# Performance work log

Hardware: AMD Instinct MI355X
Metric: run time of the kernel (lower is better)

Reference implementation:

```python
import jax, jax.numpy as jnp
import numpy as np
from jax import lax

LBDA = 0.5   # soft-min temperature from OTAM_cum_dist_v2 default
EPS = 0.01   # cos_sim epsilon


def otam_cum_dist(dists, lbda=LBDA):
    """Soft-DTW-style OTAM DP. dists: [nq, ns, L, S] -> [nq, ns].
    Faithful to OTAM_cum_dist_v2: pad last dim by (1,1) with zeros, then run the
    row-wise recurrence. Soft-min computed via stable logsumexp (same math as
    -lbda*log(sum exp(-x/lbda)))."""
    nq, ns, L, S = dists.shape
    d = jnp.pad(dists, ((0, 0), (0, 0), (0, 0), (1, 1)))  # [nq, ns, L, W], W=S+2
    W = S + 2
    # Row 0: cum[0, m] = cum[0, m-1] + d[0, m], cum[0, 0] = 0
    row0 = jnp.concatenate(
        [jnp.zeros((nq, ns, 1), d.dtype), jnp.cumsum(d[:, :, 0, 1:], axis=-1)], axis=-1)
    if L == 1:
        return row0[..., -1]

    m_idx = jnp.arange(1, W)
    include_up = (m_idx == 1) | (m_idx == W - 1)  # only first/last cols use cum[l-1, m]
    INF = jnp.asarray(jnp.inf, d.dtype)

    def row_step(prev_row, d_row):
        # prev_row, d_row: [nq, ns, W]
        xs = (
            jnp.moveaxis(d_row[:, :, 1:], -1, 0),        # d[l, m],       [W-1, nq, ns]
            jnp.moveaxis(prev_row[:, :, :-1], -1, 0),    # cum[l-1, m-1]
            jnp.moveaxis(prev_row[:, :, 1:], -1, 0),     # cum[l-1, m]
            include_up,
        )

        def col_step(cur_left, x):
            d_m, p_diag, p_up, inc = x
            up = jnp.where(inc, p_up, INF)               # masked term -> exp(-inf)=0
            terms = jnp.stack([p_diag, cur_left, up])    # [3, nq, ns]
            new = d_m - lbda * jax.nn.logsumexp(-terms / lbda, axis=0)
            return new, new

        _, cols = lax.scan(col_step, jnp.zeros((nq, ns), d.dtype), xs)
        row = jnp.concatenate(
            [jnp.zeros((nq, ns, 1), d.dtype), jnp.moveaxis(cols, 0, -1)], axis=-1)
        return row, None

    d_rows = jnp.moveaxis(d[:, :, 1:, :], 2, 0)          # [L-1, nq, ns, W]
    final_row, _ = lax.scan(row_step, row0, d_rows)
    return final_row[..., -1]


def reference(support_features, query_features):
    """OTAM meta-logits (cum_dist_g = -otam_distance) of DSN_TEMPORAL.
    support_features: [n_classes, L, D] class prototypes; query_features: [nq, L, D]."""
    nq, Lq, D = query_features.shape
    ns, Ls, _ = support_features.shape
    q = query_features.reshape(nq * Lq, D)
    s = support_features.reshape(ns * Ls, D)
    # cos_sim with epsilon in denominator (faithful to cos_sim())
    num = q @ s.T
    den = (jnp.linalg.norm(q, axis=-1)[:, None]
           * jnp.linalg.norm(s, axis=-1)[None, :] + EPS)
    frame_dists = 1.0 - num / den                         # [nq*L, ns*S]
    dists = frame_dists.reshape(nq, Lq, ns, Ls).transpose(0, 2, 1, 3)  # [nq, ns, L, S]
    cum = otam_cum_dist(dists) + otam_cum_dist(dists.transpose(0, 1, 3, 2))
    return -cum                                           # meta_logits [nq, ns]


def setup_inputs() -> dict:
    key = jax.random.key(0)
    k1, k2 = jax.random.split(key)
    return {
        "support_features": jax.random.normal(k1, (64, 8, 576), dtype=jnp.float32),
        "query_features": jax.random.normal(k2, (2048, 8, 576), dtype=jnp.float32),
    }
```

## Files before the change

kernel.cpp:

```cpp
#include <hip/hip_runtime.h>

#define D_K 576
#define NSLAB 18
#define LBDA_INV 2.0f
#define HALF_LBDA 0.5f
#define EPS 0.01f
#define DSTRIDE 136
#define SLAB_USHORTS 4096

typedef __attribute__((ext_vector_type(8))) short short8;
typedef __attribute__((ext_vector_type(4))) short short4v;
typedef __attribute__((ext_vector_type(4))) float f32x4;

__device__ inline short f2bf(float f) {
    unsigned u = __float_as_uint(f);
    u += 0x7FFF + ((u >> 16) & 1);
    return (short)(u >> 16);
}
__device__ inline float bf2f(unsigned short s) {
    return __uint_as_float(((unsigned)s) << 16);
}

__device__ inline float softmin3(float a, float b, float c) {
    float mn = fminf(a, fminf(b, c));
    float s = __expf(-LBDA_INV * (a - mn)) + __expf(-LBDA_INV * (b - mn)) +
              __expf(-LBDA_INV * (c - mn));
    return mn - HALF_LBDA * __logf(s);
}
__device__ inline float softmin2(float a, float b) {
    float mn = fminf(a, b);
    float s = __expf(-LBDA_INV * (a - mn)) + __expf(-LBDA_INV * (b - mn));
    return mn - HALF_LBDA * __logf(s);
}

template <int RS, int CS>
__device__ float otam_dp(const float* d) {
    float prev[10], cur[10];
    prev[0] = 0.f;
#pragma unroll
    for (int m = 1; m <= 8; ++m) prev[m] = prev[m - 1] + d[0 * RS + (m - 1) * CS];
    prev[9] = prev[8];
#pragma unroll
    for (int l = 1; l < 8; ++l) {
        cur[0] = 0.f;
        cur[1] = d[l * RS + 0 * CS] + softmin3(prev[0], 0.f, prev[1]);
#pragma unroll
        for (int m = 2; m <= 8; ++m)
            cur[m] = d[l * RS + (m - 1) * CS] + softmin2(prev[m - 1], cur[m - 1]);
        cur[9] = softmin3(prev[8], cur[8], prev[9]);
#pragma unroll
        for (int m = 0; m < 10; ++m) prev[m] = cur[m];
    }
    return prev[9];
}

__global__ __launch_bounds__(256, 2) void fused_kernel(
        const float* __restrict__ sup, const float* __restrict__ qry,
        float* __restrict__ out) {
    __shared__ unsigned short As0[SLAB_USHORTS], Bs0[SLAB_USHORTS];
    __shared__ unsigned short As1[SLAB_USHORTS], Bs1[SLAB_USHORTS];
    __shared__ unsigned short Ds[128 * DSTRIDE];
    __shared__ float qn_l[128], sn_l[128];

    const int t = threadIdx.x;
    const int b = blockIdx.x;
    const int xcd = b & 7, s2 = b >> 3;
    const int sblk = s2 >> 4;
    const int qblk = xcd * 16 + (s2 & 15);

    const float* qsrc = qry + (size_t)qblk * 128 * D_K;
    const float* ssrc = sup + (size_t)sblk * 128 * D_K;

    const int rr = t >> 3;
    const int cc = t & 7;
    const int c_in = cc >> 1, half = cc & 1;

    const int lane = t & 63;
    const int wave = t >> 6;
    const int wm = wave >> 1, wn = wave & 1;
    const int col16 = lane & 15, quad = lane >> 4;

    f32x4 acc[4][4];
#pragma unroll
    for (int i = 0; i < 4; ++i)
#pragma unroll
        for (int j = 0; j < 4; ++j) acc[i][j] = (f32x4){0.f, 0.f, 0.f, 0.f};

    int aoff[4], boff[4], woff[4];
#pragma unroll
    for (int mt = 0; mt < 4; ++mt)
        aoff[mt] = (quad * 128 + ((wm * 64 + mt * 16 + col16) ^ (quad << 1))) * 8;
#pragma unroll
    for (int nt = 0; nt < 4; ++nt)
        boff[nt] = (quad * 128 + ((wn * 64 + nt * 16 + col16) ^ (quad << 1))) * 8;
#pragma unroll
    for (int i = 0; i < 4; ++i)
        woff[i] = (c_in * 128 + ((i * 32 + rr) ^ (c_in << 1))) * 8 + half * 4;

    float ssA[4] = {0.f, 0.f, 0.f, 0.f}, ssB[4] = {0.f, 0.f, 0.f, 0.f};
    float4 va[4], vb[4];

    auto stage_load = [&](int sl) {
        const int off = sl * 32 + cc * 4;
#pragma unroll
        for (int i = 0; i < 4; ++i) {
            va[i] = *(const float4*)(qsrc + (size_t)(i * 32 + rr) * D_K + off);
            vb[i] = *(const float4*)(ssrc + (size_t)(i * 32 + rr) * D_K + off);
        }
    };
    auto stage_write = [&](unsigned short* __restrict__ A,
                           unsigned short* __restrict__ B) {
#pragma unroll
        for (int i = 0; i < 4; ++i) {
            ssA[i] += va[i].x * va[i].x + va[i].y * va[i].y +
                      va[i].z * va[i].z + va[i].w * va[i].w;
            ssB[i] += vb[i].x * vb[i].x + vb[i].y * vb[i].y +
                      vb[i].z * vb[i].z + vb[i].w * vb[i].w;
            short4v oa = {f2bf(va[i].x), f2bf(va[i].y), f2bf(va[i].z), f2bf(va[i].w)};
            short4v ob = {f2bf(vb[i].x), f2bf(vb[i].y), f2bf(vb[i].z), f2bf(vb[i].w)};
            *(short4v*)(&A[woff[i]]) = oa;
            *(short4v*)(&B[woff[i]]) = ob;
        }
    };
    auto compute = [&](const unsigned short* __restrict__ A,
                       const unsigned short* __restrict__ B) {
        short8 af[4], bq[4];
#pragma unroll
        for (int mt = 0; mt < 4; ++mt) af[mt] = *(const short8*)(&A[aoff[mt]]);
#pragma unroll
        for (int nt = 0; nt < 4; ++nt) bq[nt] = *(const short8*)(&B[boff[nt]]);
#pragma unroll
        for (int mt = 0; mt < 4; ++mt)
#pragma unroll
            for (int nt = 0; nt < 4; ++nt)
                acc[mt][nt] = __builtin_amdgcn_mfma_f32_16x16x32_bf16(
                    af[mt], bq[nt], acc[mt][nt], 0, 0, 0);
    };

    stage_load(0);
    stage_write(As0, Bs0);
    __syncthreads();

#pragma unroll 1
    for (int sp = 0; sp < 9; ++sp) {
        stage_load(2 * sp + 1);
        compute(As0, Bs0);
        stage_write(As1, Bs1);
        __syncthreads();
        if (sp < 8) stage_load(2 * sp + 2);
        compute(As1, Bs1);
        if (sp < 8) stage_write(As0, Bs0);
        __syncthreads();
    }

#pragma unroll
    for (int i = 0; i < 4; ++i) {
        float a = ssA[i], s = ssB[i];
        a += __shfl_down(a, 4); a += __shfl_down(a, 2); a += __shfl_down(a, 1);
        s += __shfl_down(s, 4); s += __shfl_down(s, 2); s += __shfl_down(s, 1);
        if ((t & 7) == 0) {
            qn_l[i * 32 + rr] = sqrtf(a);
            sn_l[i * 32 + rr] = sqrtf(s);
        }
    }
    __syncthreads();

#pragma unroll
    for (int mt = 0; mt < 4; ++mt) {
#pragma unroll
        for (int reg = 0; reg < 4; ++reg) {
            int m = wm * 64 + mt * 16 + quad * 4 + reg;
            float qv = qn_l[m];
#pragma unroll
            for (int nt = 0; nt < 4; ++nt) {
                int n = wn * 64 + nt * 16 + col16;
                float sv = sn_l[n];
                float dist = 1.f - acc[mt][nt][reg] * __builtin_amdgcn_rcpf(qv * sv + EPS);
                Ds[m * DSTRIDE + n] = (unsigned short)f2bf(dist);
            }
        }
    }
    __syncthreads();

    const int ql = t >> 4, sj = t & 15;
    float d[64];
#pragma unroll
    for (int l = 0; l < 8; ++l) {
        short8 rowv = *(const short8*)(&Ds[(ql * 8 + l) * DSTRIDE + sj * 8]);
#pragma unroll
        for (int j = 0; j < 8; ++j) d[l * 8 + j] = bf2f((unsigned short)rowv[j]);
    }
    float r1 = otam_dp<8, 1>(d);
    float r2 = otam_dp<1, 8>(d);
    int qg = qblk * 16 + ql, sg = sblk * 16 + sj;
    out[qg * 64 + sg] = -(r1 + r2);
}

extern "C" void kernel_launch(void* const* d_in, const int* in_sizes, int n_in,
                              void* d_out, int out_size, void* d_ws, size_t ws_size,
                              hipStream_t stream) {
    const float* sup = (const float*)d_in[0];
    const float* qry = (const float*)d_in[1];
    float* out = (float*)d_out;
    (void)d_ws; (void)ws_size;
    fused_kernel<<<dim3(512), dim3(256), 0, stream>>>(sup, qry, out);
}
```

Measured before the change: 105.4 us.

## Halve query tile, alias LDS pool, split OTAM directions across thread halves

Each block now covers 64 query frames instead of 128 and the grid doubles to 1024 blocks. The staging buffers, distance tile and a new transposed distance tile share one aliased LDS pool, and launch bounds ask for 4 blocks per CU. The two OTAM DP passes (row-wise and column-wise) now run in separate halves of the block, reading rows straight from LDS instead of holding 64 floats in registers, and combine through shared memory. This aims to raise occupancy and parallelism in the latency-bound DP stage, at the cost of reloading the support tile twice as often and adding an extra transposed store and a barrier.

```diff
diff --git a/kernel.cpp b/kernel.cpp
--- a/kernel.cpp
+++ b/kernel.cpp
@@ -6,7 +6,8 @@
 #define HALF_LBDA 0.5f
 #define EPS 0.01f
 #define DSTRIDE 136
-#define SLAB_USHORTS 4096
+#define DT_STRIDE 72
+#define POOL_USHORTS 17920
 
 typedef __attribute__((ext_vector_type(8))) short short8;
 typedef __attribute__((ext_vector_type(4))) short short4v;
@@ -33,20 +34,27 @@
     return mn - HALF_LBDA * __logf(s);
 }
 
-template <int RS, int CS>
-__device__ float otam_dp(const float* d) {
-    float prev[10], cur[10];
+template <int STRIDE>
+__device__ float otam_dp_rows(const unsigned short* base) {
+    float x[8], prev[10], cur[10];
+    auto load_row = [&](int l) {
+        short8 v = *(const short8*)(base + l * STRIDE);
+#pragma unroll
+        for (int j = 0; j < 8; ++j) x[j] = bf2f((unsigned short)v[j]);
+    };
+    load_row(0);
     prev[0] = 0.f;
 #pragma unroll
-    for (int m = 1; m <= 8; ++m) prev[m] = prev[m - 1] + d[0 * RS + (m - 1) * CS];
+    for (int m = 1; m <= 8; ++m) prev[m] = prev[m - 1] + x[m - 1];
     prev[9] = prev[8];
 #pragma unroll
     for (int l = 1; l < 8; ++l) {
+        load_row(l);
         cur[0] = 0.f;
-        cur[1] = d[l * RS + 0 * CS] + softmin3(prev[0], 0.f, prev[1]);
+        cur[1] = x[0] + softmin3(prev[0], 0.f, prev[1]);
 #pragma unroll
         for (int m = 2; m <= 8; ++m)
-            cur[m] = d[l * RS + (m - 1) * CS] + softmin2(prev[m - 1], cur[m - 1]);
+            cur[m] = x[m - 1] + softmin2(prev[m - 1], cur[m - 1]);
         cur[9] = softmin3(prev[8], cur[8], prev[9]);
 #pragma unroll
         for (int m = 0; m < 10; ++m) prev[m] = cur[m];
@@ -54,21 +62,25 @@
     return prev[9];
 }
 
-__global__ __launch_bounds__(256, 2) void fused_kernel(
+__global__ __launch_bounds__(256, 4) void fused_kernel(
         const float* __restrict__ sup, const float* __restrict__ qry,
         float* __restrict__ out) {
-    __shared__ unsigned short As0[SLAB_USHORTS], Bs0[SLAB_USHORTS];
-    __shared__ unsigned short As1[SLAB_USHORTS], Bs1[SLAB_USHORTS];
-    __shared__ unsigned short Ds[128 * DSTRIDE];
-    __shared__ float qn_l[128], sn_l[128];
+    __shared__ __align__(16) unsigned short pool[POOL_USHORTS];
+    __shared__ float qn_l[64], sn_l[128];
+    unsigned short* const As0 = pool;
+    unsigned short* const Bs0 = pool + 2048;
+    unsigned short* const As1 = pool + 6144;
+    unsigned short* const Bs1 = pool + 8192;
+    unsigned short* const Ds  = pool;
+    unsigned short* const DsT = pool + 8704;
 
     const int t = threadIdx.x;
     const int b = blockIdx.x;
     const int xcd = b & 7, s2 = b >> 3;
-    const int sblk = s2 >> 4;
-    const int qblk = xcd * 16 + (s2 & 15);
-
-    const float* qsrc = qry + (size_t)qblk * 128 * D_K;
+    const int sblk = s2 >> 5;
+    const int qh = xcd * 32 + (s2 & 31);
+
+    const float* qsrc = qry + (size_t)qh * 64 * D_K;
     const float* ssrc = sup + (size_t)sblk * 128 * D_K;
 
     const int rr = t >> 3;
@@ -80,57 +92,68 @@
     const int wm = wave >> 1, wn = wave & 1;
     const int col16 = lane & 15, quad = lane >> 4;
 
-    f32x4 acc[4][4];
-#pragma unroll
-    for (int i = 0; i < 4; ++i)
+    f32x4 acc[2][4];
+#pragma unroll
+    for (int i = 0; i < 2; ++i)
 #pragma unroll
         for (int j = 0; j < 4; ++j) acc[i][j] = (f32x4){0.f, 0.f, 0.f, 0.f};
 
-    int aoff[4], boff[4], woff[4];
-#pragma unroll
-    for (int mt = 0; mt < 4; ++mt)
-        aoff[mt] = (quad * 128 + ((wm * 64 + mt * 16 + col16) ^ (quad << 1))) * 8;
-#pragma unroll
-    for (int nt = 0; nt < 4; ++nt)
-        boff[nt] = (quad * 128 + ((wn * 64 + nt * 16 + col16) ^ (quad << 1))) * 8;
-#pragma unroll
-    for (int i = 0; i < 4; ++i)
-        woff[i] = (c_in * 128 + ((i * 32 + rr) ^ (c_in << 1))) * 8 + half * 4;
-
-    float ssA[4] = {0.f, 0.f, 0.f, 0.f}, ssB[4] = {0.f, 0.f, 0.f, 0.f};
-    float4 va[4], vb[4];
+    int aoff[2], boff[4], woffA[2], woffB[4];
+#pragma unroll
+    for (int mt = 0; mt < 2; ++mt) {
+        int m = wm * 32 + mt * 16 + col16;
+        aoff[mt] = (quad * 64 + (m ^ (quad << 1))) * 8;
+    }
+#pragma unroll
+    for (int nt = 0; nt < 4; ++nt) {
+        int n = wn * 64 + nt * 16 + col16;
+        boff[nt] = (quad * 128 + (n ^ (quad << 1))) * 8;
+    }
+#pragma unroll
+    for (int j = 0; j < 2; ++j)
+        woffA[j] = (c_in * 64 + ((j * 32 + rr) ^ (c_in << 1))) * 8 + half * 4;
+#pragma unroll
+    for (int j = 0; j < 4; ++j)
+        woffB[j] = (c_in * 128 + ((j * 32 + rr) ^ (c_in << 1))) * 8 + half * 4;
+
+    float ssA[2] = {0.f, 0.f}, ssB[4] = {0.f, 0.f, 0.f, 0.f};
+    float4 va[2], vb[4];
 
     auto stage_load = [&](int sl) {
         const int off = sl * 32 + cc * 4;
 #pragma unroll
-        for (int i = 0; i < 4; ++i) {
-            va[i] = *(const float4*)(qsrc + (size_t)(i * 32 + rr) * D_K + off);
-            vb[i] = *(const float4*)(ssrc + (size_t)(i * 32 + rr) * D_K + off);
-        }
+        for (int j = 0; j < 2; ++j)
+            va[j] = *(const float4*)(qsrc + (size_t)(j * 32 + rr) * D_K + off);
+#pragma unroll
+        for (int j = 0; j < 4; ++j)
+            vb[j] = *(const float4*)(ssrc + (size_t)(j * 32 + rr) * D_K + off);
     };
     auto stage_write = [&](unsigned short* __restrict__ A,
                            unsigned short* __restrict__ B) {
 #pragma unroll
-        for (int i = 0; i < 4; ++i) {
-            ssA[i] += va[i].x * va[i].x + va[i].y * va[i].y +
-                      va[i].z * va[i].z + va[i].w * va[i].w;
-            ssB[i] += vb[i].x * vb[i].x + vb[i].y * vb[i].y +
-                      vb[i].z * vb[i].z + vb[i].w * vb[i].w;
-            short4v oa = {f2bf(va[i].x), f2bf(va[i].y), f2bf(va[i].z), f2bf(va[i].w)};
-            short4v ob = {f2bf(vb[i].x), f2bf(vb[i].y), f2bf(vb[i].z), f2bf(vb[i].w)};
-            *(short4v*)(&A[woff[i]]) = oa;
-            *(short4v*)(&B[woff[i]]) = ob;
+        for (int j = 0; j < 2; ++j) {
+            ssA[j] += va[j].x * va[j].x + va[j].y * va[j].y +
+                      va[j].z * va[j].z + va[j].w * va[j].w;
+            short4v oa = {f2bf(va[j].x), f2bf(va[j].y), f2bf(va[j].z), f2bf(va[j].w)};
+            *(short4v*)(&A[woffA[j]]) = oa;
+        }
+#pragma unroll
+        for (int j = 0; j < 4; ++j) {
+            ssB[j] += vb[j].x * vb[j].x + vb[j].y * vb[j].y +
+                      vb[j].z * vb[j].z + vb[j].w * vb[j].w;
+            short4v ob = {f2bf(vb[j].x), f2bf(vb[j].y), f2bf(vb[j].z), f2bf(vb[j].w)};
+            *(short4v*)(&B[woffB[j]]) = ob;
         }
     };
     auto compute = [&](const unsigned short* __restrict__ A,
                        const unsigned short* __restrict__ B) {
-        short8 af[4], bq[4];
-#pragma unroll
-        for (int mt = 0; mt < 4; ++mt) af[mt] = *(const short8*)(&A[aoff[mt]]);
+        short8 af[2], bq[4];
+#pragma unroll
+        for (int mt = 0; mt < 2; ++mt) af[mt] = *(const short8*)(&A[aoff[mt]]);
 #pragma unroll
         for (int nt = 0; nt < 4; ++nt) bq[nt] = *(const short8*)(&B[boff[nt]]);
 #pragma unroll
-        for (int mt = 0; mt < 4; ++mt)
+        for (int mt = 0; mt < 2; ++mt)
 #pragma unroll
             for (int nt = 0; nt < 4; ++nt)
                 acc[mt][nt] = __builtin_amdgcn_mfma_f32_16x16x32_bf16(
@@ -154,46 +177,51 @@
     }
 
 #pragma unroll
-    for (int i = 0; i < 4; ++i) {
-        float a = ssA[i], s = ssB[i];
+    for (int j = 0; j < 2; ++j) {
+        float a = ssA[j];
         a += __shfl_down(a, 4); a += __shfl_down(a, 2); a += __shfl_down(a, 1);
+        if ((t & 7) == 0) qn_l[j * 32 + rr] = sqrtf(a);
+    }
+#pragma unroll
+    for (int j = 0; j < 4; ++j) {
+        float s = ssB[j];
         s += __shfl_down(s, 4); s += __shfl_down(s, 2); s += __shfl_down(s, 1);
-        if ((t & 7) == 0) {
-            qn_l[i * 32 + rr] = sqrtf(a);
-            sn_l[i * 32 + rr] = sqrtf(s);
-        }
-    }
-    __syncthreads();
-
-#pragma unroll
-    for (int mt = 0; mt < 4; ++mt) {
+        if ((t & 7) == 0) sn_l[j * 32 + rr] = sqrtf(s);
+    }
+    __syncthreads();
+
+#pragma unroll
+    for (int mt = 0; mt < 2; ++mt) {
 #pragma unroll
         for (int reg = 0; reg < 4; ++reg) {
-            int m = wm * 64 + mt * 16 + quad * 4 + reg;
+            int m = wm * 32 + mt * 16 + quad * 4 + reg;
             float qv = qn_l[m];
 #pragma unroll
             for (int nt = 0; nt < 4; ++nt) {
                 int n = wn * 64 + nt * 16 + col16;
                 float sv = sn_l[n];
                 float dist = 1.f - acc[mt][nt][reg] * __builtin_amdgcn_rcpf(qv * sv + EPS);
-                Ds[m * DSTRIDE + n] = (unsigned short)f2bf(dist);
+                unsigned short h = (unsigned short)f2bf(dist);
+                Ds[m * DSTRIDE + n] = h;
+                DsT[n * DT_STRIDE + m] = h;
             }
         }
     }
     __syncthreads();
 
-    const int ql = t >> 4, sj = t & 15;
-    float d[64];
-#pragma unroll
-    for (int l = 0; l < 8; ++l) {
-        short8 rowv = *(const short8*)(&Ds[(ql * 8 + l) * DSTRIDE + sj * 8]);
-#pragma unroll
-        for (int j = 0; j < 8; ++j) d[l * 8 + j] = bf2f((unsigned short)rowv[j]);
-    }
-    float r1 = otam_dp<8, 1>(d);
-    float r2 = otam_dp<1, 8>(d);
-    int qg = qblk * 16 + ql, sg = sblk * 16 + sj;
-    out[qg * 64 + sg] = -(r1 + r2);
+    const int p = t & 127, ql = p >> 4, sj = p & 15;
+    float r;
+    if (t < 128) {
+        r = otam_dp_rows<DSTRIDE>(Ds + (ql * 8) * DSTRIDE + sj * 8);
+    } else {
+        r = otam_dp_rows<DT_STRIDE>(DsT + (sj * 8) * DT_STRIDE + ql * 8);
+        sn_l[p] = r;
+    }
+    __syncthreads();
+    if (t < 128) {
+        int qg = qh * 8 + ql, sg = sblk * 16 + sj;
+        out[qg * 64 + sg] = -(r + sn_l[p]);
+    }
 }
 
 extern "C" void kernel_launch(void* const* d_in, const int* in_sizes, int n_in,
@@ -203,5 +231,5 @@
     const float* qry = (const float*)d_in[1];
     float* out = (float*)d_out;
     (void)d_ws; (void)ws_size;
-    fused_kernel<<<dim3(512), dim3(256), 0, stream>>>(sup, qry, out);
-}
+    fused_kernel<<<dim3(1024), dim3(256), 0, stream>>>(sup, qry, out);
+}
```

After: 110.3 us. 1.05x slower.
